# Kernel optimization log

Hardware: AMD Instinct MI355X
Metric: run time of the kernel (lower is better)

The kernel has to match this reference:

```python
import jax, jax.numpy as jnp
import numpy as np

B, S, P, D = 4, 2, 1024, 1024   # batch, sample_count, seq (== n_ctx), d_embed
I, H = 16, 64                   # n_heads, d_head
ALPHA = 1.0                     # weight_alpha


def setup_inputs() -> dict:
    key = jax.random.key(0)
    kx, kk, kq, kv, ko = jax.random.split(key, 5)
    scale = ALPHA / np.sqrt(D)
    return {
        "x": jax.random.normal(kx, (B, S, P, D), dtype=jnp.float32),
        "W_K": (scale * jax.random.normal(kk, (S, I, H, D))).astype(jnp.float32),
        "W_Q": (scale * jax.random.normal(kq, (S, I, H, D))).astype(jnp.float32),
        "W_V": (scale * jax.random.normal(kv, (S, I, H, D))).astype(jnp.float32),
        "W_O": (scale * jax.random.normal(ko, (S, D, I * H))).astype(jnp.float32),
    }


def reference(x, W_K, W_Q, W_V, W_O):
    # x: [b, s, p, d]; W_{K,Q,V}: [s, i, h, d]; W_O: [s, d, i*h]
    k = jnp.einsum('sihd,bspd->bsiph', W_K, x)
    q = jnp.einsum('sihd,bspd->bsiph', W_Q, x)
    v = jnp.einsum('sihd,bspd->bsiph', W_V, x)
    # scores: [b, s, i, q, p] (query rows, key cols)
    scores = jnp.einsum('bsiph,bsiqh->bsiqp', k, q)
    p = x.shape[-2]
    mask = jnp.tril(jnp.ones((p, p), dtype=x.dtype))  # causal lower-triangular
    # faithful to torch: tril(scores) - 1e10 * (1 - mask), scaled AFTER masking
    masked = scores * mask - 1.0e10 * (1.0 - mask)
    attn = jax.nn.softmax(masked / np.sqrt(H), axis=-1)
    z = jnp.einsum('bsiph,bsiqp->bsiqh', v, attn)      # [b, s, i, q, h]
    b = x.shape[0]
    z_flat = jnp.transpose(z, (0, 1, 3, 2, 4)).reshape(b, S, p, I * H)  # b s q (i h)
    out = jnp.einsum('sdf,bsqf->bsqd', W_O, z_flat)
    return out
```

## Files before the change

### kernel.cpp

```cpp
#include <hip/hip_runtime.h>
#include <hip/hip_bf16.h>
#include <cmath>

#define C_B 4
#define C_S 2
#define C_P 1024
#define C_D 1024
#define C_I 16
#define C_H 64

typedef unsigned short u16;
typedef unsigned int u32;
typedef __attribute__((ext_vector_type(8))) short short8;
typedef __attribute__((ext_vector_type(8))) __bf16 bf16x8;
typedef __attribute__((ext_vector_type(4))) float f32x4;
typedef __attribute__((ext_vector_type(16))) float f32x16;
typedef __attribute__((ext_vector_type(4))) u32 u32x4;

__device__ __forceinline__ u16 f2bf(float f) {
  union { float f; unsigned u; } c; c.f = f;
  unsigned u = c.u;
  u += 0x7fffu + ((u >> 16) & 1u);
  return (u16)(u >> 16);
}

__device__ __forceinline__ u32 cvtpk_bf16(float lo, float hi) {
  u32 r;
  asm("v_cvt_pk_bf16_f32 %0, %1, %2" : "=v"(r) : "v"(lo), "v"(hi));
  return r;
}

__device__ __forceinline__ float fexp2(float x) {
  return __builtin_amdgcn_exp2f(x);
}

__device__ __forceinline__ f32x4 mfma16(short8 a, short8 b, f32x4 c) {
  return __builtin_amdgcn_mfma_f32_16x16x32_bf16(
      __builtin_bit_cast(bf16x8, a), __builtin_bit_cast(bf16x8, b), c, 0, 0, 0);
}

__device__ __forceinline__ f32x16 mfma32(short8 a, short8 b, f32x16 c) {
  return __builtin_amdgcn_mfma_f32_32x32x16_bf16(
      __builtin_bit_cast(bf16x8, a), __builtin_bit_cast(bf16x8, b), c, 0, 0, 0);
}

__device__ __forceinline__ void load_lds16(const u16* g, u16* l) {
  __builtin_amdgcn_global_load_lds(
      (const __attribute__((address_space(1))) void*)g,
      (__attribute__((address_space(3))) void*)l, 16, 0, 0);
}

__global__ void cvt_all(const float* __restrict__ x,
                        const float* __restrict__ wq, const float* __restrict__ wk,
                        const float* __restrict__ wvp, const float* __restrict__ wo,
                        u16* __restrict__ xbf, u16* __restrict__ wall,
                        u16* __restrict__ wob) {
  const int b = blockIdx.x;
  if (b < 2048) {
    int i = b * 256 + threadIdx.x;
    const int n4 = (C_B * C_S * C_P * C_D) / 4, stride = 2048 * 256;
    for (; i < n4; i += stride) {
      float4 v = reinterpret_cast<const float4*>(x)[i];
      ushort4 o;
      o.x = f2bf(v.x); o.y = f2bf(v.y); o.z = f2bf(v.z); o.w = f2bf(v.w);
      reinterpret_cast<ushort4*>(xbf)[i] = o;
    }
  } else {
    const int j = b - 2048;
    const int t = j >> 9;
    const float* src = (t == 0) ? wq : (t == 1) ? wk : (t == 2) ? wvp : wo;
    int i = (j & 511) * 256 + threadIdx.x;
    const int stride = 512 * 256;
    for (; i < 524288; i += stride) {
      float4 v = reinterpret_cast<const float4*>(src)[i];
      ushort4 o;
      o.x = f2bf(v.x); o.y = f2bf(v.y); o.z = f2bf(v.z); o.w = f2bf(v.w);
      if (t < 3) {
        int s = i >> 18;
        int rem = i & 262143;
        reinterpret_cast<ushort4*>(wall)[s * 786432 + t * 262144 + rem] = o;
      } else {
        reinterpret_cast<ushort4*>(wob)[i] = o;
      }
    }
  }
}

template<int MODE>
__global__ __launch_bounds__(512, 2)
void gemm_bt(const u16* __restrict__ A, const u16* __restrict__ Bm, void* __restrict__ C) {
  __shared__ __align__(16) u16 lds[49152];
  const int tid = threadIdx.x;
  const int lane = tid & 63;
  const int wv = tid >> 6;
  const int wr = wv >> 2, wc = wv & 3;
  const int lr = lane & 15, lg = lane >> 4;

  const int h = (int)blockIdx.x;
  const int lid = (MODE == 3) ? ((h & 7) * 96 + (h >> 3)) : ((h & 7) * 32 + (h >> 3));
  const int bs  = (MODE == 3) ? (lid / 96) : (lid >> 5);
  const int r2  = (MODE == 3) ? (lid % 96) : (lid & 31);
  const int by = r2 >> 2, bx = r2 & 3;
  const int m0 = bx * 256, n0 = by * 128;

  const u16* Ab = A + (size_t)bs * (C_P * C_D);
  const u16* Bb = Bm + (size_t)(bs & 1) * (MODE == 3 ? 3 * 1048576 : 1048576);
  f32x4 acc[8][2] = {};

#define STAGE(T, BUF)                                                           \
  {                                                                             \
    const int kof = (T) * 64;                                                   \
    _Pragma("unroll")                                                           \
    for (int i = 0; i < 6; ++i) {                                               \
      int cid = tid + i * 512;                                                  \
      if (i < 4) {                                                              \
        int row = cid >> 3, c8 = (cid & 7) ^ (row & 7);                         \
        load_lds16(Ab + (size_t)(m0 + row) * 1024 + kof + c8 * 8,               \
                   lds + (BUF) * 16384 + cid * 8);                              \
      } else {                                                                  \
        int c2 = cid - 2048;                                                    \
        int row = c2 >> 3, c8 = (c2 & 7) ^ (row & 7);                           \
        load_lds16(Bb + (size_t)(n0 + row) * 1024 + kof + c8 * 8,               \
                   lds + 32768 + (BUF) * 8192 + c2 * 8);                        \
      }                                                                         \
    }                                                                           \
  }

  STAGE(0, 0)

  for (int t = 0; t < 16; ++t) {
    const int bbuf = t & 1;
    __builtin_amdgcn_s_barrier();
    if (t < 15) {
      STAGE(t + 1, bbuf ^ 1)
      asm volatile("s_waitcnt vmcnt(6)" ::: "memory");
    } else {
      asm volatile("s_waitcnt vmcnt(0)" ::: "memory");
    }
    __builtin_amdgcn_s_barrier();

    const char* Als = (const char*)lds + bbuf * 32768;
    const char* Bls = (const char*)lds + 65536 + bbuf * 16384;
#pragma unroll
    for (int p = 0; p < 4; ++p) {
      short8 af[2][2], bfr[2][2];
#pragma unroll
      for (int m2 = 0; m2 < 2; ++m2)
#pragma unroll
        for (int ks = 0; ks < 2; ++ks) {
          int row = wr * 128 + (p * 2 + m2) * 16 + lr;
          af[m2][ks] = *reinterpret_cast<const short8*>(
              Als + row * 128 + (((ks << 6) | (lg << 4)) ^ ((row & 7) << 4)));
        }
#pragma unroll
      for (int nf = 0; nf < 2; ++nf)
#pragma unroll
        for (int ks = 0; ks < 2; ++ks) {
          int row = wc * 32 + nf * 16 + lr;
          bfr[nf][ks] = *reinterpret_cast<const short8*>(
              Bls + row * 128 + (((ks << 6) | (lg << 4)) ^ ((row & 7) << 4)));
        }
      __builtin_amdgcn_s_setprio(1);
#pragma unroll
      for (int m2 = 0; m2 < 2; ++m2)
#pragma unroll
        for (int nf = 0; nf < 2; ++nf)
#pragma unroll
          for (int ks = 0; ks < 2; ++ks)
            acc[p * 2 + m2][nf] = mfma16(af[m2][ks], bfr[nf][ks], acc[p * 2 + m2][nf]);
      __builtin_amdgcn_s_setprio(0);
    }
  }
#undef STAGE

  if (MODE == 2) {
    float* dst = (float*)C + (size_t)bs * (C_P * C_D);
#pragma unroll
    for (int mf = 0; mf < 8; ++mf)
#pragma unroll
      for (int nf = 0; nf < 2; ++nf)
#pragma unroll
        for (int r = 0; r < 4; ++r) {
          int p = m0 + wr * 128 + mf * 16 + lg * 4 + r;
          int col = n0 + wc * 32 + nf * 16 + lr;
          dst[(size_t)p * C_D + col] = acc[mf][nf][r];
        }
  } else {
    const int t3 = by >> 3;
    if (t3 < 2) {
      u16* dst = (u16*)C + (size_t)t3 * 8388608;
      const float scl = (t3 == 0) ? 0.18033688f : 1.0f;
#pragma unroll
      for (int mf = 0; mf < 8; ++mf)
#pragma unroll
        for (int nf = 0; nf < 2; ++nf)
#pragma unroll
          for (int r = 0; r < 4; ++r) {
            int p = m0 + wr * 128 + mf * 16 + lg * 4 + r;
            int cg = (by & 7) * 128 + wc * 32 + nf * 16 + lr;
            dst[(size_t)(bs * C_I + (cg >> 6)) * 65536 + (size_t)p * C_H + (cg & 63)] =
                f2bf(acc[mf][nf][r] * scl);
          }
    } else {
      __syncthreads();
      char* trc = (char*)lds;
#pragma unroll
      for (int mf = 0; mf < 8; ++mf)
#pragma unroll
        for (int nf = 0; nf < 2; ++nf) {
          int nl = wc * 32 + nf * 16 + lr;
          int pl0 = wr * 128 + mf * 16 + lg * 4;
#pragma unroll
          for (int r = 0; r < 4; r += 2) {
            u32 wpk = cvtpk_bf16(acc[mf][nf][r], acc[mf][nf][r + 1]);
            *reinterpret_cast<u32*>(
                trc + nl * 512 + (((pl0 + r) * 2) ^ ((nl & 15) << 5))) = wpk;
          }
        }
      __syncthreads();
      const int nl = tid >> 2, seg = tid & 3;
      const int cg = (by & 7) * 128 + nl;
      u16* dst = (u16*)C + 2 * 8388608 +
                 (size_t)(bs * C_I + (cg >> 6)) * 65536 + (size_t)(cg & 63) * C_P +
                 m0 + seg * 64;
#pragma unroll
      for (int j = 0; j < 8; ++j) {
        short8 v = *reinterpret_cast<const short8*>(
            trc + nl * 512 + ((seg * 128 + j * 16) ^ ((nl & 15) << 5)));
        *reinterpret_cast<short8*>(dst + j * 8) = v;
      }
    }
  }
}

__global__ __launch_bounds__(256, 4)
void attn_kernel(const u16* __restrict__ Q, const u16* __restrict__ K,
                 const u16* __restrict__ VT, u16* __restrict__ Z) {
  __shared__ __align__(16) u16 Kt[2][64 * 64];
  __shared__ __align__(16) u16 Vt[2][64 * 64];
  const int tid = threadIdx.x;
  const int lane = tid & 63, wv = tid >> 6;
  const int l31 = lane & 31, l5 = lane >> 5;
  const int b = (int)blockIdx.x;
  const int head = (b & 7) * 16 + ((b >> 3) & 15);
  const int y = b >> 7;
  const int qg = 7 - (y ^ (((y + 2) >> 2) & 1));
  const int bs = head >> 4, ih = head & 15;
  const int q0w = qg * 128 + wv * 32;
  const u16* Qh = Q + (size_t)head * (C_P * C_H);
  const u16* Kh = K + (size_t)head * (C_P * C_H);
  const u16* Vh = VT + (size_t)head * (C_P * C_H);
  const int ntiles = 2 * qg + 2;
  const int myq = q0w + l31;
  const int swz = (l31 & 7) << 4;

  short8 qf[4];
#pragma unroll
  for (int hk = 0; hk < 4; ++hk)
    qf[hk] = *reinterpret_cast<const short8*>(
        &Qh[(size_t)(q0w + l31) * C_H + hk * 16 + l5 * 8]);

  f32x16 zacc[2] = {};
  float mrun = -INFINITY, lrun = 0.f;

#define ASTAGE(t, buf)                                                          \
  {                                                                             \
    _Pragma("unroll")                                                           \
    for (int i = 0; i < 2; ++i) {                                               \
      int cid = wv * 128 + i * 64 + lane;                                       \
      int r = cid >> 3;                                                         \
      int sc = (cid & 7) ^ (r & 7);                                             \
      load_lds16(Kh + (size_t)((t) * 64 + r) * C_H + sc * 8, &Kt[buf][cid * 8]);\
      load_lds16(Vh + (size_t)r * C_P + (t) * 64 + sc * 8, &Vt[buf][cid * 8]);  \
    }                                                                           \
  }

  ASTAGE(0, 0)

  for (int t = 0; t < ntiles; ++t) {
    const int cur = t & 1;
    __builtin_amdgcn_s_barrier();
    if (t + 1 < ntiles) {
      ASTAGE(t + 1, cur ^ 1)
      asm volatile("s_waitcnt vmcnt(4)" ::: "memory");
    } else {
      asm volatile("s_waitcnt vmcnt(0)" ::: "memory");
    }
    __builtin_amdgcn_s_barrier();

    if (t * 64 <= q0w + 31) {
      const char* Kc = (const char*)Kt[cur];
      f32x16 sA[2];
      __builtin_amdgcn_s_setprio(1);
#pragma unroll
      for (int kt2 = 0; kt2 < 2; ++kt2) {
        f32x16 acc = {};
        int rb = (kt2 * 32 + l31) * 128 + ((l5 * 16) ^ swz);
#pragma unroll
        for (int hk = 0; hk < 4; ++hk) {
          short8 kf = *reinterpret_cast<const short8*>(Kc + (rb ^ (hk * 32)));
          acc = mfma32(kf, qf[hk], acc);
        }
        sA[kt2] = acc;
      }
      __builtin_amdgcn_s_setprio(0);

      if (t * 64 + 63 > q0w) {
#pragma unroll
        for (int kt2 = 0; kt2 < 2; ++kt2)
#pragma unroll
          for (int r = 0; r < 16; ++r) {
            int kv = t * 64 + kt2 * 32 + (r & 3) + 8 * (r >> 2) + 4 * l5;
            if (kv > myq) sA[kt2][r] = -1.8033688e9f;
          }
      }

      float tmax = sA[0][0];
#pragma unroll
      for (int r = 1; r < 16; ++r) tmax = fmaxf(tmax, sA[0][r]);
#pragma unroll
      for (int r = 0; r < 16; ++r) tmax = fmaxf(tmax, sA[1][r]);
      tmax = fmaxf(tmax, __shfl_xor(tmax, 32, 64));
      if (!__all(tmax - mrun <= 11.5416f)) {
        float mnew = fmaxf(mrun, tmax);
        float scal = fexp2(mrun - mnew);
        mrun = mnew;
        lrun *= scal;
#pragma unroll
        for (int r = 0; r < 16; ++r) {
          float sc = __shfl(scal, (r & 3) + 8 * (r >> 2) + 4 * l5, 64);
          zacc[0][r] *= sc;
          zacc[1][r] *= sc;
        }
      }
      float rsum = 0.f;
#pragma unroll
      for (int kt2 = 0; kt2 < 2; ++kt2)
#pragma unroll
        for (int r = 0; r < 16; ++r) {
          float e = fexp2(sA[kt2][r] - mrun);
          sA[kt2][r] = e;
          rsum += e;
        }
      rsum += __shfl_xor(rsum, 32, 64);
      lrun += rsum;

      short8 pa[4];
#pragma unroll
      for (int kt2 = 0; kt2 < 2; ++kt2) {
        u32 W[8];
#pragma unroll
        for (int i2 = 0; i2 < 8; ++i2)
          W[i2] = cvtpk_bf16(sA[kt2][2 * i2], sA[kt2][2 * i2 + 1]);
#pragma unroll
        for (int pr = 0; pr < 4; ++pr) {
          const int a = (pr & 1) + (pr >> 1) * 4;
          const int b2 = a + 2;
          u32 send = l5 ? W[a] : W[b2];
          u32 recv = __shfl_xor(send, 32, 64);
          u32 na = l5 ? recv : W[a];
          u32 nb = l5 ? W[b2] : recv;
          W[a] = na; W[b2] = nb;
        }
        u32x4 f0 = {W[0], W[1], W[2], W[3]};
        u32x4 f1 = {W[4], W[5], W[6], W[7]};
        pa[kt2 * 2 + 0] = __builtin_bit_cast(short8, f0);
        pa[kt2 * 2 + 1] = __builtin_bit_cast(short8, f1);
      }

      const char* Vc = (const char*)Vt[cur];
      __builtin_amdgcn_s_setprio(1);
#pragma unroll
      for (int kt = 0; kt < 4; ++kt)
#pragma unroll
        for (int ht = 0; ht < 2; ++ht) {
          int row = ht * 32 + l31;
          int vb = row * 128 + (((kt * 32) | (l5 * 16)) ^ ((row & 7) << 4));
          short8 vf = *reinterpret_cast<const short8*>(Vc + vb);
          zacc[ht] = mfma32(pa[kt], vf, zacc[ht]);
        }
      __builtin_amdgcn_s_setprio(0);
    }
  }

  float inv = 1.0f / lrun;
  u16* Zb = Z + (size_t)bs * (C_P * C_I * C_H) + ih * C_H;
#pragma unroll
  for (int r = 0; r < 16; ++r) {
    int qloc = (r & 3) + 8 * (r >> 2) + 4 * l5;
    float iv = __shfl(inv, qloc, 64);
    size_t rowo = (size_t)(q0w + qloc) * (C_I * C_H);
    Zb[rowo + l31]      = f2bf(zacc[0][r] * iv);
    Zb[rowo + 32 + l31] = f2bf(zacc[1][r] * iv);
  }
#undef ASTAGE
}

extern "C" void kernel_launch(void* const* d_in, const int* in_sizes, int n_in,
                              void* d_out, int out_size, void* d_ws, size_t ws_size,
                              hipStream_t stream) {
  const float* x  = (const float*)d_in[0];
  const float* wk = (const float*)d_in[1];
  const float* wq = (const float*)d_in[2];
  const float* wv = (const float*)d_in[3];
  const float* wo = (const float*)d_in[4];

  char* w = (char*)d_ws;
  u16* xbf  = (u16*)w;
  u16* wall = (u16*)(w + 16777216);
  u16* wob  = (u16*)(w + 29360128);
  u16* qws  = (u16*)(w + 33554432);
  u16* zws  = xbf;
  u16* kws  = qws + 8388608;
  u16* vtw  = kws + 8388608;

  cvt_all<<<4096, 256, 0, stream>>>(x, wq, wk, wv, wo, xbf, wall, wob);

  gemm_bt<3><<<768, 512, 0, stream>>>(xbf, wall, qws);

  attn_kernel<<<1024, 256, 0, stream>>>(qws, kws, vtw, zws);

  gemm_bt<2><<<256, 512, 0, stream>>>(zws, wob, d_out);
}
```

Baseline: 138.8 us.

## Switch projection GEMM to 32x32x16 MFMA with 128x256 block tiles

The projection GEMM now uses 32x32x16 bf16 MFMA instructions instead of 16x16x32, with each wave computing a 64x64 tile. The block tile changes from 256x128 (M x N) to 128x256, and the LDS staging offsets, swizzles and epilogue index math (including the V transpose path) are rewritten to match. The larger MFMA shape is meant to cut LDS fragment reads per FLOP and raise matrix throughput per instruction. In exchange, the new accumulator layouts change how the epilogue stores are laid out and how well they coalesce.

Measured after the change: 139.3 us. No clear change (+0.4%).

```diff
diff --git a/kernel.cpp b/kernel.cpp
--- a/kernel.cpp
+++ b/kernel.cpp
@@ -32,11 +32,6 @@
 
 __device__ __forceinline__ float fexp2(float x) {
   return __builtin_amdgcn_exp2f(x);
-}
-
-__device__ __forceinline__ f32x4 mfma16(short8 a, short8 b, f32x4 c) {
-  return __builtin_amdgcn_mfma_f32_16x16x32_bf16(
-      __builtin_bit_cast(bf16x8, a), __builtin_bit_cast(bf16x8, b), c, 0, 0, 0);
 }
 
 __device__ __forceinline__ f32x16 mfma32(short8 a, short8 b, f32x16 c) {
@@ -94,18 +89,18 @@
   const int lane = tid & 63;
   const int wv = tid >> 6;
   const int wr = wv >> 2, wc = wv & 3;
-  const int lr = lane & 15, lg = lane >> 4;
+  const int l31 = lane & 31, l5 = lane >> 5;
 
   const int h = (int)blockIdx.x;
   const int lid = (MODE == 3) ? ((h & 7) * 96 + (h >> 3)) : ((h & 7) * 32 + (h >> 3));
   const int bs  = (MODE == 3) ? (lid / 96) : (lid >> 5);
   const int r2  = (MODE == 3) ? (lid % 96) : (lid & 31);
-  const int by = r2 >> 2, bx = r2 & 3;
-  const int m0 = bx * 256, n0 = by * 128;
+  const int bx = r2 & 7, by = r2 >> 3;
+  const int m0 = bx * 128, n0 = by * 256;
 
   const u16* Ab = A + (size_t)bs * (C_P * C_D);
   const u16* Bb = Bm + (size_t)(bs & 1) * (MODE == 3 ? 3 * 1048576 : 1048576);
-  f32x4 acc[8][2] = {};
+  f32x16 acc[2][2] = {};
 
 #define STAGE(T, BUF)                                                           \
   {                                                                             \
@@ -113,15 +108,15 @@
     _Pragma("unroll")                                                           \
     for (int i = 0; i < 6; ++i) {                                               \
       int cid = tid + i * 512;                                                  \
-      if (i < 4) {                                                              \
+      if (i < 2) {                                                              \
         int row = cid >> 3, c8 = (cid & 7) ^ (row & 7);                         \
         load_lds16(Ab + (size_t)(m0 + row) * 1024 + kof + c8 * 8,               \
-                   lds + (BUF) * 16384 + cid * 8);                              \
+                   lds + (BUF) * 8192 + cid * 8);                               \
       } else {                                                                  \
-        int c2 = cid - 2048;                                                    \
+        int c2 = cid - 1024;                                                    \
         int row = c2 >> 3, c8 = (c2 & 7) ^ (row & 7);                           \
         load_lds16(Bb + (size_t)(n0 + row) * 1024 + kof + c8 * 8,               \
-                   lds + 32768 + (BUF) * 8192 + c2 * 8);                        \
+                   lds + 16384 + (BUF) * 16384 + c2 * 8);                       \
       }                                                                         \
     }                                                                           \
   }
@@ -139,35 +134,29 @@
     }
     __builtin_amdgcn_s_barrier();
 
-    const char* Als = (const char*)lds + bbuf * 32768;
-    const char* Bls = (const char*)lds + 65536 + bbuf * 16384;
-#pragma unroll
-    for (int p = 0; p < 4; ++p) {
-      short8 af[2][2], bfr[2][2];
-#pragma unroll
-      for (int m2 = 0; m2 < 2; ++m2)
-#pragma unroll
-        for (int ks = 0; ks < 2; ++ks) {
-          int row = wr * 128 + (p * 2 + m2) * 16 + lr;
-          af[m2][ks] = *reinterpret_cast<const short8*>(
-              Als + row * 128 + (((ks << 6) | (lg << 4)) ^ ((row & 7) << 4)));
-        }
-#pragma unroll
-      for (int nf = 0; nf < 2; ++nf)
-#pragma unroll
-        for (int ks = 0; ks < 2; ++ks) {
-          int row = wc * 32 + nf * 16 + lr;
-          bfr[nf][ks] = *reinterpret_cast<const short8*>(
-              Bls + row * 128 + (((ks << 6) | (lg << 4)) ^ ((row & 7) << 4)));
-        }
+    const u16* Ael = lds + bbuf * 8192;
+    const u16* Bel = lds + 16384 + bbuf * 16384;
+#pragma unroll
+    for (int ks = 0; ks < 4; ++ks) {
+      short8 am[2], bn[2];
+#pragma unroll
+      for (int mw = 0; mw < 2; ++mw) {
+        int row = wr * 64 + mw * 32 + l31;
+        int ch = (ks * 2 + l5) ^ (row & 7);
+        am[mw] = *reinterpret_cast<const short8*>(Ael + row * 64 + ch * 8);
+      }
+#pragma unroll
+      for (int nw = 0; nw < 2; ++nw) {
+        int row = wc * 64 + nw * 32 + l31;
+        int ch = (ks * 2 + l5) ^ (row & 7);
+        bn[nw] = *reinterpret_cast<const short8*>(Bel + row * 64 + ch * 8);
+      }
       __builtin_amdgcn_s_setprio(1);
 #pragma unroll
-      for (int m2 = 0; m2 < 2; ++m2)
-#pragma unroll
-        for (int nf = 0; nf < 2; ++nf)
-#pragma unroll
-          for (int ks = 0; ks < 2; ++ks)
-            acc[p * 2 + m2][nf] = mfma16(af[m2][ks], bfr[nf][ks], acc[p * 2 + m2][nf]);
+      for (int mw = 0; mw < 2; ++mw)
+#pragma unroll
+        for (int nw = 0; nw < 2; ++nw)
+          acc[mw][nw] = mfma32(am[mw], bn[nw], acc[mw][nw]);
       __builtin_amdgcn_s_setprio(0);
     }
   }
@@ -176,58 +165,59 @@
   if (MODE == 2) {
     float* dst = (float*)C + (size_t)bs * (C_P * C_D);
 #pragma unroll
-    for (int mf = 0; mf < 8; ++mf)
-#pragma unroll
-      for (int nf = 0; nf < 2; ++nf)
-#pragma unroll
-        for (int r = 0; r < 4; ++r) {
-          int p = m0 + wr * 128 + mf * 16 + lg * 4 + r;
-          int col = n0 + wc * 32 + nf * 16 + lr;
-          dst[(size_t)p * C_D + col] = acc[mf][nf][r];
+    for (int mw = 0; mw < 2; ++mw)
+#pragma unroll
+      for (int nw = 0; nw < 2; ++nw)
+#pragma unroll
+        for (int r = 0; r < 16; ++r) {
+          int p = m0 + wr * 64 + mw * 32 + (r & 3) + 8 * (r >> 2) + 4 * l5;
+          int col = n0 + wc * 64 + nw * 32 + l31;
+          dst[(size_t)p * C_D + col] = acc[mw][nw][r];
         }
   } else {
-    const int t3 = by >> 3;
+    const int t3 = by >> 2;
     if (t3 < 2) {
       u16* dst = (u16*)C + (size_t)t3 * 8388608;
       const float scl = (t3 == 0) ? 0.18033688f : 1.0f;
 #pragma unroll
-      for (int mf = 0; mf < 8; ++mf)
-#pragma unroll
-        for (int nf = 0; nf < 2; ++nf)
-#pragma unroll
-          for (int r = 0; r < 4; ++r) {
-            int p = m0 + wr * 128 + mf * 16 + lg * 4 + r;
-            int cg = (by & 7) * 128 + wc * 32 + nf * 16 + lr;
+      for (int mw = 0; mw < 2; ++mw)
+#pragma unroll
+        for (int nw = 0; nw < 2; ++nw)
+#pragma unroll
+          for (int r = 0; r < 16; ++r) {
+            int p = m0 + wr * 64 + mw * 32 + (r & 3) + 8 * (r >> 2) + 4 * l5;
+            int cg = (by & 3) * 256 + wc * 64 + nw * 32 + l31;
             dst[(size_t)(bs * C_I + (cg >> 6)) * 65536 + (size_t)p * C_H + (cg & 63)] =
-                f2bf(acc[mf][nf][r] * scl);
+                f2bf(acc[mw][nw][r] * scl);
           }
     } else {
       __syncthreads();
       char* trc = (char*)lds;
 #pragma unroll
-      for (int mf = 0; mf < 8; ++mf)
-#pragma unroll
-        for (int nf = 0; nf < 2; ++nf) {
-          int nl = wc * 32 + nf * 16 + lr;
-          int pl0 = wr * 128 + mf * 16 + lg * 4;
-#pragma unroll
-          for (int r = 0; r < 4; r += 2) {
-            u32 wpk = cvtpk_bf16(acc[mf][nf][r], acc[mf][nf][r + 1]);
+      for (int mw = 0; mw < 2; ++mw)
+#pragma unroll
+        for (int nw = 0; nw < 2; ++nw) {
+          int nl = wc * 64 + nw * 32 + l31;
+#pragma unroll
+          for (int r = 0; r < 16; r += 2) {
+            int pl = wr * 64 + mw * 32 + (r & 3) + 8 * (r >> 2) + 4 * l5;
+            int pl2 = pl * 2;
+            u32 wpk = cvtpk_bf16(acc[mw][nw][r], acc[mw][nw][r + 1]);
             *reinterpret_cast<u32*>(
-                trc + nl * 512 + (((pl0 + r) * 2) ^ ((nl & 15) << 5))) = wpk;
+                trc + nl * 256 + ((((pl2 >> 4) ^ (nl & 15)) << 4) | (pl2 & 15))) = wpk;
           }
         }
       __syncthreads();
-      const int nl = tid >> 2, seg = tid & 3;
-      const int cg = (by & 7) * 128 + nl;
+      const int nl = tid >> 1, seg = tid & 1;
+      const int cg = (by & 3) * 256 + nl;
       u16* dst = (u16*)C + 2 * 8388608 +
-                 (size_t)(bs * C_I + (cg >> 6)) * 65536 + (size_t)(cg & 63) * C_P +
-                 m0 + seg * 64;
+                 (size_t)(bs * C_I + (cg >> 6)) * 65536 + (size_t)(cg & 63) * C_P + m0;
 #pragma unroll
       for (int j = 0; j < 8; ++j) {
+        int c = seg * 8 + j;
         short8 v = *reinterpret_cast<const short8*>(
-            trc + nl * 512 + ((seg * 128 + j * 16) ^ ((nl & 15) << 5)));
-        *reinterpret_cast<short8*>(dst + j * 8) = v;
+            trc + nl * 256 + ((c ^ (nl & 15)) << 4));
+        *reinterpret_cast<short8*>(dst + c * 8) = v;
       }
     }
   }
```

## Split QKV projection into dedicated 256x256-tile GEMM with half-step LDS pipelining

Applied to the files above, without the earlier changes.

Replaces the templated GEMM for the QKV projection with a dedicated kernel that uses 256x256 output tiles (384 blocks instead of 768), a 128KB LDS footprint at one block per CU, and an MFMA-fragment-ordered LDS layout. K-halves are staged separately and interleaved with MFMA groups, so global-to-LDS loads overlap compute within each iteration. The larger tile raises arithmetic intensity and cuts redundant loads of A and B. In exchange it lowers occupancy and block count, which can leave CUs underused, and it adds register pressure from 32 accumulator fragments.

New measurement: 152.3 us. 9.7% more time.

```diff
diff --git a/kernel.cpp b/kernel.cpp
--- a/kernel.cpp
+++ b/kernel.cpp
@@ -86,9 +86,175 @@
   }
 }
 
-template<int MODE>
+__global__ __launch_bounds__(512, 1)
+void gemm_qkv(const u16* __restrict__ A, const u16* __restrict__ Bm, void* __restrict__ C) {
+  __shared__ __align__(16) u16 lds[65536];
+  const int tid = threadIdx.x;
+  const int lane = tid & 63;
+  const int wv = tid >> 6;
+  const int wr = wv >> 2, wc = wv & 3;
+  const int lr = lane & 15, lg = lane >> 4;
+
+  const int h = (int)blockIdx.x;
+  const int lid = (h & 7) * 48 + (h >> 3);
+  const int bsi = lid / 48;
+  const int r2 = lid % 48;
+  const int bx = r2 & 3, by = r2 >> 2;
+  const int m0 = bx * 256, n0 = by * 256;
+
+  const u16* Ab = A + (size_t)bsi * (C_P * C_D);
+  const u16* Bb = Bm + (size_t)(bsi & 1) * (3 * 1048576);
+  f32x4 acc[8][4] = {};
+
+#define STAGE_A(T, BUF, KS)                                                     \
+  {                                                                             \
+    const int kof = (T) * 64;                                                   \
+    u16* lb = lds + (BUF) * 32768;                                              \
+    _Pragma("unroll")                                                           \
+    for (int i2 = 0; i2 < 2; ++i2) {                                            \
+      int o2 = tid + i2 * 512;                                                  \
+      int mf = o2 >> 6, w2 = o2 & 63;                                           \
+      load_lds16(Ab + (size_t)(m0 + mf * 16 + (w2 & 15)) * 1024 + kof +         \
+                     (KS) * 32 + (w2 >> 4) * 8,                                 \
+                 lb + (mf * 2 + (KS)) * 512 + w2 * 8);                          \
+    }                                                                           \
+  }
+#define STAGE_B(T, BUF, KS)                                                     \
+  {                                                                             \
+    const int kof = (T) * 64;                                                   \
+    u16* lb = lds + (BUF) * 32768 + 16384;                                      \
+    _Pragma("unroll")                                                           \
+    for (int i2 = 0; i2 < 2; ++i2) {                                            \
+      int o2 = tid + i2 * 512;                                                  \
+      int nf = o2 >> 6, w2 = o2 & 63;                                           \
+      load_lds16(Bb + (size_t)(n0 + nf * 16 + (w2 & 15)) * 1024 + kof +         \
+                     (KS) * 32 + (w2 >> 4) * 8,                                 \
+                 lb + (nf * 2 + (KS)) * 512 + w2 * 8);                          \
+    }                                                                           \
+  }
+
+  STAGE_A(0, 0, 0) STAGE_B(0, 0, 0) STAGE_A(0, 0, 1) STAGE_B(0, 0, 1)
+  STAGE_A(1, 1, 0) STAGE_B(1, 1, 0)
+
+  for (int t = 0; t < 16; ++t) {
+    if (t < 15) {
+      asm volatile("s_waitcnt vmcnt(4)" ::: "memory");
+    } else {
+      asm volatile("s_waitcnt vmcnt(0)" ::: "memory");
+    }
+    __builtin_amdgcn_s_barrier();
+
+    const u16* Ael = lds + (t & 1) * 32768;
+    const u16* Bel = Ael + 16384;
+    short8 am[4], bn[4];
+
+#pragma unroll
+    for (int i = 0; i < 4; ++i)
+      am[i] = *reinterpret_cast<const short8*>(Ael + ((wr * 8 + i) * 2 + 0) * 512 + lane * 8);
+#pragma unroll
+    for (int i = 0; i < 4; ++i)
+      bn[i] = *reinterpret_cast<const short8*>(Bel + ((wc * 4 + i) * 2 + 0) * 512 + lane * 8);
+    if (t + 1 < 16) STAGE_A(t + 1, (t ^ 1) & 1, 1)
+    __builtin_amdgcn_s_setprio(1);
+#pragma unroll
+    for (int i = 0; i < 4; ++i)
+#pragma unroll
+      for (int j = 0; j < 4; ++j)
+        acc[i][j] = mfma16(am[i], bn[j], acc[i][j]);
+    __builtin_amdgcn_s_setprio(0);
+
+#pragma unroll
+    for (int i = 0; i < 4; ++i)
+      am[i] = *reinterpret_cast<const short8*>(Ael + ((wr * 8 + 4 + i) * 2 + 0) * 512 + lane * 8);
+    if (t + 1 < 16) STAGE_B(t + 1, (t ^ 1) & 1, 1)
+    __builtin_amdgcn_s_setprio(1);
+#pragma unroll
+    for (int i = 0; i < 4; ++i)
+#pragma unroll
+      for (int j = 0; j < 4; ++j)
+        acc[4 + i][j] = mfma16(am[i], bn[j], acc[4 + i][j]);
+    __builtin_amdgcn_s_setprio(0);
+
+    __builtin_amdgcn_s_barrier();
+
+#pragma unroll
+    for (int i = 0; i < 4; ++i)
+      am[i] = *reinterpret_cast<const short8*>(Ael + ((wr * 8 + i) * 2 + 1) * 512 + lane * 8);
+#pragma unroll
+    for (int i = 0; i < 4; ++i)
+      bn[i] = *reinterpret_cast<const short8*>(Bel + ((wc * 4 + i) * 2 + 1) * 512 + lane * 8);
+    if (t + 2 < 16) STAGE_A(t + 2, t & 1, 0)
+    __builtin_amdgcn_s_setprio(1);
+#pragma unroll
+    for (int i = 0; i < 4; ++i)
+#pragma unroll
+      for (int j = 0; j < 4; ++j)
+        acc[i][j] = mfma16(am[i], bn[j], acc[i][j]);
+    __builtin_amdgcn_s_setprio(0);
+
+#pragma unroll
+    for (int i = 0; i < 4; ++i)
+      am[i] = *reinterpret_cast<const short8*>(Ael + ((wr * 8 + 4 + i) * 2 + 1) * 512 + lane * 8);
+    if (t + 2 < 16) STAGE_B(t + 2, t & 1, 0)
+    __builtin_amdgcn_s_setprio(1);
+#pragma unroll
+    for (int i = 0; i < 4; ++i)
+#pragma unroll
+      for (int j = 0; j < 4; ++j)
+        acc[4 + i][j] = mfma16(am[i], bn[j], acc[4 + i][j]);
+    __builtin_amdgcn_s_setprio(0);
+  }
+#undef STAGE_A
+#undef STAGE_B
+
+  const int t3 = by >> 2;
+  if (t3 < 2) {
+    u16* dst = (u16*)C + (size_t)t3 * 8388608;
+    const float scl = (t3 == 0) ? 0.18033688f : 1.0f;
+#pragma unroll
+    for (int mf = 0; mf < 8; ++mf)
+#pragma unroll
+      for (int nf = 0; nf < 4; ++nf)
+#pragma unroll
+        for (int r = 0; r < 4; ++r) {
+          int p = m0 + wr * 128 + mf * 16 + lg * 4 + r;
+          int cg = (by & 3) * 256 + wc * 64 + nf * 16 + lr;
+          dst[(size_t)(bsi * C_I + (cg >> 6)) * 65536 + (size_t)p * C_H + (cg & 63)] =
+              f2bf(acc[mf][nf][r] * scl);
+        }
+  } else {
+    __syncthreads();
+    char* trc = (char*)lds;
+#pragma unroll
+    for (int mf = 0; mf < 8; ++mf)
+#pragma unroll
+      for (int nf = 0; nf < 4; ++nf) {
+        int nl = wc * 64 + nf * 16 + lr;
+#pragma unroll
+        for (int r = 0; r < 4; r += 2) {
+          int pl = wr * 128 + mf * 16 + lg * 4 + r;
+          u32 wpk = cvtpk_bf16(acc[mf][nf][r], acc[mf][nf][r + 1]);
+          *reinterpret_cast<u32*>(
+              trc + nl * 512 + ((((pl >> 3) ^ (nl & 15)) << 4) | ((pl * 2) & 15))) = wpk;
+        }
+      }
+    __syncthreads();
+    const int nl = tid >> 1, seg = tid & 1;
+    const int cg = (by & 3) * 256 + nl;
+    u16* dst = (u16*)C + 2 * 8388608 +
+               (size_t)(bsi * C_I + (cg >> 6)) * 65536 + (size_t)(cg & 63) * C_P + m0;
+#pragma unroll
+    for (int j = 0; j < 16; ++j) {
+      int c = seg * 16 + j;
+      short8 v = *reinterpret_cast<const short8*>(
+          trc + nl * 512 + ((c ^ (nl & 15)) << 4));
+      *reinterpret_cast<short8*>(dst + c * 8) = v;
+    }
+  }
+}
+
 __global__ __launch_bounds__(512, 2)
-void gemm_bt(const u16* __restrict__ A, const u16* __restrict__ Bm, void* __restrict__ C) {
+void gemm_out(const u16* __restrict__ A, const u16* __restrict__ Bm, float* __restrict__ C) {
   __shared__ __align__(16) u16 lds[49152];
   const int tid = threadIdx.x;
   const int lane = tid & 63;
@@ -97,17 +263,17 @@
   const int lr = lane & 15, lg = lane >> 4;
 
   const int h = (int)blockIdx.x;
-  const int lid = (MODE == 3) ? ((h & 7) * 96 + (h >> 3)) : ((h & 7) * 32 + (h >> 3));
-  const int bs  = (MODE == 3) ? (lid / 96) : (lid >> 5);
-  const int r2  = (MODE == 3) ? (lid % 96) : (lid & 31);
+  const int lid = (h & 7) * 32 + (h >> 3);
+  const int bsi = lid >> 5;
+  const int r2 = lid & 31;
   const int by = r2 >> 2, bx = r2 & 3;
   const int m0 = bx * 256, n0 = by * 128;
 
-  const u16* Ab = A + (size_t)bs * (C_P * C_D);
-  const u16* Bb = Bm + (size_t)(bs & 1) * (MODE == 3 ? 3 * 1048576 : 1048576);
+  const u16* Ab = A + (size_t)bsi * (C_P * C_D);
+  const u16* Bb = Bm + (size_t)(bsi & 1) * 1048576;
   f32x4 acc[8][2] = {};
 
-#define STAGE(T, BUF)                                                           \
+#define STAGEO(T, BUF)                                                          \
   {                                                                             \
     const int kof = (T) * 64;                                                   \
     _Pragma("unroll")                                                           \
@@ -126,13 +292,13 @@
     }                                                                           \
   }
 
-  STAGE(0, 0)
+  STAGEO(0, 0)
 
   for (int t = 0; t < 16; ++t) {
     const int bbuf = t & 1;
     __builtin_amdgcn_s_barrier();
     if (t < 15) {
-      STAGE(t + 1, bbuf ^ 1)
+      STAGEO(t + 1, bbuf ^ 1)
       asm volatile("s_waitcnt vmcnt(6)" ::: "memory");
     } else {
       asm volatile("s_waitcnt vmcnt(0)" ::: "memory");
@@ -171,66 +337,19 @@
       __builtin_amdgcn_s_setprio(0);
     }
   }
-#undef STAGE
-
-  if (MODE == 2) {
-    float* dst = (float*)C + (size_t)bs * (C_P * C_D);
-#pragma unroll
-    for (int mf = 0; mf < 8; ++mf)
-#pragma unroll
-      for (int nf = 0; nf < 2; ++nf)
-#pragma unroll
-        for (int r = 0; r < 4; ++r) {
-          int p = m0 + wr * 128 + mf * 16 + lg * 4 + r;
-          int col = n0 + wc * 32 + nf * 16 + lr;
-          dst[(size_t)p * C_D + col] = acc[mf][nf][r];
-        }
-  } else {
-    const int t3 = by >> 3;
-    if (t3 < 2) {
-      u16* dst = (u16*)C + (size_t)t3 * 8388608;
-      const float scl = (t3 == 0) ? 0.18033688f : 1.0f;
-#pragma unroll
-      for (int mf = 0; mf < 8; ++mf)
-#pragma unroll
-        for (int nf = 0; nf < 2; ++nf)
-#pragma unroll
-          for (int r = 0; r < 4; ++r) {
-            int p = m0 + wr * 128 + mf * 16 + lg * 4 + r;
-            int cg = (by & 7) * 128 + wc * 32 + nf * 16 + lr;
-            dst[(size_t)(bs * C_I + (cg >> 6)) * 65536 + (size_t)p * C_H + (cg & 63)] =
-                f2bf(acc[mf][nf][r] * scl);
-          }
-    } else {
-      __syncthreads();
-      char* trc = (char*)lds;
-#pragma unroll
-      for (int mf = 0; mf < 8; ++mf)
-#pragma unroll
-        for (int nf = 0; nf < 2; ++nf) {
-          int nl = wc * 32 + nf * 16 + lr;
-          int pl0 = wr * 128 + mf * 16 + lg * 4;
-#pragma unroll
-          for (int r = 0; r < 4; r += 2) {
-            u32 wpk = cvtpk_bf16(acc[mf][nf][r], acc[mf][nf][r + 1]);
-            *reinterpret_cast<u32*>(
-                trc + nl * 512 + (((pl0 + r) * 2) ^ ((nl & 15) << 5))) = wpk;
-          }
-        }
-      __syncthreads();
-      const int nl = tid >> 2, seg = tid & 3;
-      const int cg = (by & 7) * 128 + nl;
-      u16* dst = (u16*)C + 2 * 8388608 +
-                 (size_t)(bs * C_I + (cg >> 6)) * 65536 + (size_t)(cg & 63) * C_P +
-                 m0 + seg * 64;
-#pragma unroll
-      for (int j = 0; j < 8; ++j) {
-        short8 v = *reinterpret_cast<const short8*>(
-            trc + nl * 512 + ((seg * 128 + j * 16) ^ ((nl & 15) << 5)));
-        *reinterpret_cast<short8*>(dst + j * 8) = v;
-      }
-    }
-  }
+#undef STAGEO
+
+  float* dst = C + (size_t)bsi * (C_P * C_D);
+#pragma unroll
+  for (int mf = 0; mf < 8; ++mf)
+#pragma unroll
+    for (int nf = 0; nf < 2; ++nf)
+#pragma unroll
+      for (int r = 0; r < 4; ++r) {
+        int p = m0 + wr * 128 + mf * 16 + lg * 4 + r;
+        int col = n0 + wc * 32 + nf * 16 + lr;
+        dst[(size_t)p * C_D + col] = acc[mf][nf][r];
+      }
 }
 
 __global__ __launch_bounds__(256, 4)
@@ -416,9 +535,9 @@
 
   cvt_all<<<4096, 256, 0, stream>>>(x, wq, wk, wv, wo, xbf, wall, wob);
 
-  gemm_bt<3><<<768, 512, 0, stream>>>(xbf, wall, qws);
+  gemm_qkv<<<384, 512, 0, stream>>>(xbf, wall, qws);
 
   attn_kernel<<<1024, 256, 0, stream>>>(qws, kws, vtw, zws);
 
-  gemm_bt<2><<<256, 512, 0, stream>>>(zws, wob, d_out);
-}
+  gemm_out<<<256, 512, 0, stream>>>(zws, wob, (float*)d_out);
+}
```
